# Performance work log

Measured on AMD Instinct MI355X. Metric: run time of the kernel, lower is better.

Reference implementation:

```python
import jax, jax.numpy as jnp
import numpy as np

B, V, J = 1024, 6890, 24
P_FEAT = (J - 1) * 9  # 207 pose-blendshape features
SMPL_PARENTS = [-1, 0, 0, 0, 1, 2, 3, 4, 5, 6, 7, 8, 9, 9, 9, 12, 13, 14, 16, 17, 18, 19, 20, 21]


def setup_inputs() -> dict:
    key = jax.random.key(0)
    ks = jax.random.split(key, 7)
    return {
        "betas": jax.random.normal(ks[0], (B, 10), jnp.float32),
        "full_pose": jax.random.normal(ks[1], (B, 72), jnp.float32) * 0.3,
        "v_template": jax.random.normal(ks[2], (1, V, 3), jnp.float32),
        "shapedirs": jax.random.normal(ks[3], (V, 3, 10), jnp.float32) * 0.01,
        "posedirs": jax.random.normal(ks[4], (P_FEAT, V * 3), jnp.float32) * 0.01,
        "J_regressor": jax.nn.softmax(jax.random.normal(ks[5], (J, V), jnp.float32), axis=-1),
        "lbs_weights": jax.nn.softmax(jax.random.normal(ks[6], (V, J), jnp.float32) * 4.0, axis=-1),
        "parents": jnp.array(SMPL_PARENTS, dtype=jnp.int32),
    }


def batch_rodrigues(rot_vecs):
    # rot_vecs: [..., 3] axis-angle -> [..., 3, 3] rotation matrices
    angle = jnp.linalg.norm(rot_vecs + 1e-8, axis=-1, keepdims=True)  # [...,1]
    axis = rot_vecs / angle
    s = jnp.sin(angle)[..., None]
    c = jnp.cos(angle)[..., None]
    kx, ky, kz = axis[..., 0], axis[..., 1], axis[..., 2]
    zeros = jnp.zeros_like(kx)
    K = jnp.stack([zeros, -kz, ky, kz, zeros, -kx, -ky, kx, zeros], axis=-1)
    K = K.reshape(rot_vecs.shape[:-1] + (3, 3))
    eye = jnp.eye(3, dtype=rot_vecs.dtype)
    return eye + s * K + (1.0 - c) * (K @ K)


def reference(betas, full_pose, v_template, shapedirs, posedirs, J_regressor, lbs_weights, parents):
    p = [int(x) for x in np.asarray(jax.device_get(parents))]  # static kinematic tree
    b = betas.shape[0]

    # 1) shape blendshapes: minimal shape
    v_shaped = v_template + jnp.einsum("bl,vkl->bvk", betas, shapedirs)  # [B,V,3]

    # 2) rest joints
    J_rest = jnp.einsum("jv,bvk->bjk", J_regressor, v_shaped)  # [B,J,3]

    # 3) pose rotations + pose blendshapes
    rot_mats = batch_rodrigues(full_pose.reshape(b, J, 3))  # [B,J,3,3]
    eye = jnp.eye(3, dtype=rot_mats.dtype)
    pose_feature = (rot_mats[:, 1:] - eye).reshape(b, P_FEAT)  # [B,207]
    v_posed = v_shaped + (pose_feature @ posedirs).reshape(b, V, 3)

    # 4) kinematic chain (sequential composition over fixed 24 joints)
    rel_joints = J_rest.at[:, 1:].add(-J_rest[:, np.array(p[1:])])  # [B,J,3]
    Tm = jnp.zeros((b, J, 4, 4), dtype=rot_mats.dtype)
    Tm = Tm.at[:, :, :3, :3].set(rot_mats)
    Tm = Tm.at[:, :, :3, 3].set(rel_joints)
    Tm = Tm.at[:, :, 3, 3].set(1.0)
    chain = [Tm[:, 0]]
    for i in range(1, J):
        chain.append(chain[p[i]] @ Tm[:, i])
    transforms = jnp.stack(chain, axis=1)  # [B,J,4,4]

    J_posed = transforms[:, :, :3, 3]  # [B,J,3]

    # relative bone transforms: subtract rotated rest joints from translation
    RJ = jnp.einsum("bjmn,bjn->bjm", transforms[:, :, :3, :3], J_rest)
    A = transforms.at[:, :, :3, 3].add(-RJ)  # [B,J,4,4]

    # 5) linear blend skinning: per-vertex weighted transform then apply
    T = jnp.einsum("vj,bjmn->bvmn", lbs_weights, A)  # [B,V,4,4]
    verts = jnp.einsum("bvmn,bvn->bvm", T[:, :, :3, :3], v_posed) + T[:, :, :3, 3]

    return verts, J_posed, J_rest, A, v_shaped
```

## Files before the change

kernel.cpp:

```cpp
#include <hip/hip_runtime.h>
#include <hip/hip_bf16.h>

#define BDIM 1024
#define VDIM 6890
#define NJ   24
#define NCOL (VDIM*3)
#define KPAD 224
#define NPAD 20736
#define NB   8
#define VPAD 6912

#define OUT_VERTS   0
#define OUT_JPOSED  21166080
#define OUT_JREST   21239808
#define OUT_A       21313536
#define OUT_VSHAPED 21706752

#define SCRF_PDT    0
#define SCRF_PF     2322432
#define SCRF_JTJS   2437120

#define WSB_PDT   0u
#define WSB_PF    9289728u
#define WSB_JTJS  9748480u
#define WSB_WHI   9752064u
#define WSB_WLO   10194432u
#define WSB_AHI   10636800u
#define WSB_ALO   11685376u
#define WS_NEED   12733952u

typedef __hip_bfloat16 bf16;
typedef unsigned short ushort_t;
typedef __attribute__((ext_vector_type(8))) short  short8;
typedef __attribute__((ext_vector_type(4))) float  float4v;

__device__ __forceinline__ bf16  tob(float x) { return __float2bfloat16(x); }

__device__ __forceinline__ ushort_t bf16_rne(float x) {
    unsigned u = __builtin_bit_cast(unsigned, x);
    unsigned r = (u + 0x7FFFu + ((u >> 16) & 1u)) >> 16;
    return (ushort_t)r;
}
__device__ __forceinline__ float bf16_to_f(ushort_t h) {
    unsigned u = ((unsigned)h) << 16;
    return __builtin_bit_cast(float, u);
}

__global__ __launch_bounds__(256) void k_prep(const float* __restrict__ jreg,
        const float* __restrict__ vt, const float* __restrict__ sd,
        const float* __restrict__ lbs, float* __restrict__ jtjs,
        ushort_t* __restrict__ whi, ushort_t* __restrict__ wlo) {
    if (blockIdx.x >= 24) {
        if (!whi) return;
        int idx = (blockIdx.x - 24)*256 + threadIdx.x;
        if (idx >= VPAD*32) return;
        int v = idx >> 5, j = idx & 31;
        float x = (v < VDIM && j < 24) ? lbs[v*24 + j] : 0.f;
        ushort_t h = bf16_rne(x);
        whi[idx] = h;
        wlo[idx] = bf16_rne(x - bf16_to_f(h));
        return;
    }
    int j = blockIdx.x;
    int tid = threadIdx.x;
    float acc[33];
#pragma unroll
    for (int i = 0; i < 33; i++) acc[i] = 0.f;
    for (int v = tid; v < VDIM; v += 256) {
        float r = jreg[j*VDIM + v];
#pragma unroll
        for (int m = 0; m < 3; m++) {
            acc[m] += r * vt[v*3+m];
#pragma unroll
            for (int l = 0; l < 10; l++)
                acc[3 + m*10 + l] += r * sd[(v*3+m)*10 + l];
        }
    }
    __shared__ float red[4][33];
    int lane = tid & 63, wid = tid >> 6;
#pragma unroll
    for (int i = 0; i < 33; i++) {
        float x = acc[i];
        for (int off = 32; off > 0; off >>= 1) x += __shfl_down(x, off);
        if (lane == 0) red[wid][i] = x;
    }
    __syncthreads();
    if (tid < 33)
        jtjs[j*33 + tid] = red[0][tid] + red[1][tid] + red[2][tid] + red[3][tid];
}

__global__ __launch_bounds__(256) void k_transpose(const float* __restrict__ pd,
        bf16* __restrict__ pdt) {
    __shared__ bf16 tile[32][65];
    int nt = blockIdx.x * 64;
    int kt = blockIdx.y * 32;
    int t = threadIdx.x;
    for (int i = t; i < 32*64; i += 256) {
        int kk = i >> 6, nn = i & 63;
        int k = kt + kk, n = nt + nn;
        float v = 0.f;
        if (k < 207 && n < NCOL) v = pd[k*NCOL + n];
        tile[kk][nn] = tob(v);
    }
    __syncthreads();
    for (int i = t; i < 32*64; i += 256) {
        int kk = i & 31, nn = i >> 5;
        pdt[(nt + nn)*KPAD + kt + kk] = tile[kk][nn];
    }
}

__global__ __launch_bounds__(64) void k_pose(const float* __restrict__ betas,
        const float* __restrict__ pose, const int* __restrict__ parents,
        const float* __restrict__ jtjs, float* __restrict__ out,
        bf16* __restrict__ wspf, ushort_t* __restrict__ ahi,
        ushort_t* __restrict__ alo) {
    int b = blockIdx.x, t = threadIdx.x;
    __shared__ float R[24][9];
    __shared__ float jrest[24][3];
    __shared__ float rel[24][3];
    __shared__ float ch[24][12];
    __shared__ int par[24];
    if (t < 24) {
        par[t] = parents[t];
        float rx = pose[b*72 + t*3 + 0];
        float ry = pose[b*72 + t*3 + 1];
        float rz = pose[b*72 + t*3 + 2];
        float ax = rx + 1e-8f, ay = ry + 1e-8f, az = rz + 1e-8f;
        float angle = sqrtf(ax*ax + ay*ay + az*az);
        float inv = 1.0f / angle;
        float kx = rx*inv, ky = ry*inv, kz = rz*inv;
        float s = sinf(angle), c = cosf(angle);
        float t1 = 1.0f - c;
        float q = kx*kx + ky*ky + kz*kz;
        R[t][0] = 1.f + t1*(kx*kx - q);
        R[t][1] = -s*kz + t1*kx*ky;
        R[t][2] =  s*ky + t1*kx*kz;
        R[t][3] =  s*kz + t1*kx*ky;
        R[t][4] = 1.f + t1*(ky*ky - q);
        R[t][5] = -s*kx + t1*ky*kz;
        R[t][6] = -s*ky + t1*kx*kz;
        R[t][7] =  s*kx + t1*ky*kz;
        R[t][8] = 1.f + t1*(kz*kz - q);
    }
    __syncthreads();
    for (int i = t; i < KPAD; i += 64) {
        float pf = 0.f;
        if (i < 207) {
            int j = i/9 + 1, e = i - (j-1)*9;
            pf = R[j][e] - ((e == 0 || e == 4 || e == 8) ? 1.f : 0.f);
        }
        wspf[b*KPAD + i] = tob(pf);
    }
    for (int i = t; i < 72; i += 64) {
        int j = i/3, k = i - j*3;
        const float* JJ = &jtjs[j*33];
        float s = JJ[k];
#pragma unroll
        for (int l = 0; l < 10; l++) s += JJ[3 + k*10 + l] * betas[b*10 + l];
        jrest[j][k] = s;
        out[OUT_JREST + b*72 + i] = s;
    }
    __syncthreads();
    for (int i = t; i < 72; i += 64) {
        int j = i/3, k = i - j*3;
        rel[j][k] = jrest[j][k] - (j > 0 ? jrest[par[j]][k] : 0.f);
    }
    __syncthreads();
    if (t < 12) {
        int m = t >> 2, n = t & 3;
        ch[0][t] = (n < 3) ? R[0][m*3+n] : rel[0][m];
    }
    __syncthreads();
    for (int i = 1; i < 24; i++) {
        float val = 0.f;
        if (t < 12) {
            int m = t >> 2, n = t & 3;
            int p = par[i];
            if (n < 3)
                val = ch[p][m*4+0]*R[i][n] + ch[p][m*4+1]*R[i][3+n] + ch[p][m*4+2]*R[i][6+n];
            else
                val = ch[p][m*4+0]*rel[i][0] + ch[p][m*4+1]*rel[i][1]
                    + ch[p][m*4+2]*rel[i][2] + ch[p][m*4+3];
        }
        if (t < 12) ch[i][t] = val;
        __syncthreads();
    }
    for (int i = t; i < 72; i += 64) {
        int j = i/3, k = i - j*3;
        out[OUT_JPOSED + b*72 + i] = ch[j][k*4+3];
    }
    for (int i = t; i < 384; i += 64) {
        int j = i >> 4, e = i & 15, m = e >> 2, n = e & 3;
        float v;
        if (m < 3) {
            if (n < 3) v = ch[j][m*4+n];
            else v = ch[j][m*4+3] - (ch[j][m*4+0]*jrest[j][0] + ch[j][m*4+1]*jrest[j][1]
                                   + ch[j][m*4+2]*jrest[j][2]);
        } else v = (n == 3) ? 1.f : 0.f;
        out[OUT_A + b*384 + i] = v;
    }
    if (ahi) {
        for (int i = t; i < 512; i += 64) {
            int e = i >> 5, j = i & 31;
            float v = 0.f;
            if (j < 24 && e < 12) {
                int m = e >> 2, n = e & 3;
                if (n < 3) v = ch[j][m*4+n];
                else v = ch[j][m*4+3] - (ch[j][m*4+0]*jrest[j][0] + ch[j][m*4+1]*jrest[j][1]
                                       + ch[j][m*4+2]*jrest[j][2]);
            }
            ushort_t h = bf16_rne(v);
            ahi[b*512 + i] = h;
            alo[b*512 + i] = bf16_rne(v - bf16_to_f(h));
        }
    }
}

__global__ __launch_bounds__(256) void k_gemmlbs(const bf16* __restrict__ wspf,
        const bf16* __restrict__ wspdt, const float* __restrict__ betas,
        const float* __restrict__ sd, const float* __restrict__ vt,
        const ushort_t* __restrict__ whi, const ushort_t* __restrict__ wlo,
        const ushort_t* __restrict__ ahi, const ushort_t* __restrict__ alo,
        float* __restrict__ out) {
    __shared__ float dtile[32][260];
    const ushort_t* pf  = (const ushort_t*)wspf;
    const ushort_t* pdt = (const ushort_t*)wspdt;
    int tid  = threadIdx.x;
    int lane = tid & 63, wave = tid >> 6;
    int l15 = lane & 15, quad = lane >> 4;
    int m0 = blockIdx.y * 32;
    int v0 = blockIdx.x * 64;
    int cb = wave * 48;
    int colb = v0*3 + cb;

    {
        float4v acc[2][3] = {};
        for (int c = 0; c < 7; c++) {
            short8 a[2], bb[3];
#pragma unroll
            for (int mf = 0; mf < 2; mf++)
                a[mf] = *reinterpret_cast<const short8*>(pf + (m0 + mf*16 + l15)*KPAD + c*32 + quad*8);
#pragma unroll
            for (int nf = 0; nf < 3; nf++)
                bb[nf] = *reinterpret_cast<const short8*>(pdt + (colb + nf*16 + l15)*KPAD + c*32 + quad*8);
#pragma unroll
            for (int mf = 0; mf < 2; mf++)
#pragma unroll
                for (int nf = 0; nf < 3; nf++)
                    acc[mf][nf] = __builtin_amdgcn_mfma_f32_16x16x32_bf16(a[mf], bb[nf], acc[mf][nf], 0, 0, 0);
        }
#pragma unroll
        for (int nf = 0; nf < 3; nf++) {
            int c0 = cb + nf*16 + l15;
            int vv = c0 / 3, rr = c0 - vv*3;
            int ad = vv*4 + rr;
#pragma unroll
            for (int mf = 0; mf < 2; mf++)
#pragma unroll
                for (int r = 0; r < 4; r++)
                    dtile[mf*16 + quad*4 + r][ad] = acc[mf][nf][r];
        }
    }
    __syncthreads();

    int wv = __builtin_amdgcn_readfirstlane(wave);
    int v = v0 + lane;
    float* vsh = out + OUT_VSHAPED;
    if (v < VDIM) {
        float vtv[3];
#pragma unroll
        for (int m = 0; m < 3; m++) vtv[m] = vt[v*3 + m];
        float sdv[30];
#pragma unroll
        for (int i = 0; i < 30; i++) sdv[i] = sd[v*30 + i];
#pragma unroll 2
        for (int bb2 = 0; bb2 < 8; bb2++) {
            int b  = m0 + wv*8 + bb2;
            int bl = wv*8 + bb2;
            float vs[3];
#pragma unroll
            for (int m = 0; m < 3; m++) {
                float s = vtv[m];
#pragma unroll
                for (int l = 0; l < 10; l++) s += betas[b*10 + l] * sdv[m*10 + l];
                vs[m] = s;
            }
            float4v* slot = reinterpret_cast<float4v*>(&dtile[bl][lane*4]);
            float4v d = *slot;
            float4v vp;
            vp[0] = vs[0] + d[0]; vp[1] = vs[1] + d[1];
            vp[2] = vs[2] + d[2]; vp[3] = 0.f;
            *slot = vp;
            int base = b*NCOL + v*3;
#pragma unroll
            for (int n = 0; n < 3; n++) vsh[base + n] = vs[n];
        }
    }

    short8 bhi[4], blo[4];
#pragma unroll
    for (int nf = 0; nf < 4; nf++) {
        int vv = v0 + nf*16 + l15;
        bhi[nf] = *reinterpret_cast<const short8*>(whi + vv*32 + quad*8);
        blo[nf] = *reinterpret_cast<const short8*>(wlo + vv*32 + quad*8);
    }
    const ushort_t* ah = ahi + (size_t)(m0 + wv*8)*512 + l15*32 + quad*8;
    const ushort_t* al = alo + (size_t)(m0 + wv*8)*512 + l15*32 + quad*8;
#pragma unroll 1
    for (int g = 0; g < 2; g++) {
        short8 a_hi[4], a_lo[4];
#pragma unroll
        for (int k = 0; k < 4; k++) {
            a_hi[k] = *reinterpret_cast<const short8*>(ah + (size_t)(g*4 + k)*512);
            a_lo[k] = *reinterpret_cast<const short8*>(al + (size_t)(g*4 + k)*512);
        }
#pragma unroll
        for (int k = 0; k < 4; k++) {
            int bb2 = g*4 + k;
            int b  = m0 + wv*8 + bb2;
            int bl = wv*8 + bb2;
#pragma unroll
            for (int nf = 0; nf < 4; nf++) {
                float4v acc = {};
                acc = __builtin_amdgcn_mfma_f32_16x16x32_bf16(a_hi[k], bhi[nf], acc, 0, 0, 0);
                acc = __builtin_amdgcn_mfma_f32_16x16x32_bf16(a_lo[k], bhi[nf], acc, 0, 0, 0);
                acc = __builtin_amdgcn_mfma_f32_16x16x32_bf16(a_hi[k], blo[nf], acc, 0, 0, 0);
                int vl = nf*16 + l15;
                float4v vp = *reinterpret_cast<const float4v*>(&dtile[bl][vl*4]);
                if (quad < 3 && v0 + vl < VDIM) {
                    float o = acc[3] + acc[0]*vp[0] + acc[1]*vp[1] + acc[2]*vp[2];
                    out[(size_t)b*NCOL + (size_t)(v0 + vl)*3 + quad] = o;
                }
            }
        }
    }
}

__global__ __launch_bounds__(256) void k_posegemm(const bf16* __restrict__ wspf,
        const bf16* __restrict__ wspdt, float* __restrict__ dout) {
    const ushort_t* pf  = (const ushort_t*)wspf;
    const ushort_t* pdt = (const ushort_t*)wspdt;
    int lane = threadIdx.x & 63;
    int wave = threadIdx.x >> 6;
    int l15 = lane & 15, quad = lane >> 4;
    int m0 = blockIdx.y * 32;
    int n0 = blockIdx.x * 256 + wave * 64;
    float4v acc[2][4] = {};
    for (int c = 0; c < 7; c++) {
        short8 a[2], bb[4];
#pragma unroll
        for (int mf = 0; mf < 2; mf++)
            a[mf] = *reinterpret_cast<const short8*>(pf + (m0 + mf*16 + l15)*KPAD + c*32 + quad*8);
#pragma unroll
        for (int nf = 0; nf < 4; nf++)
            bb[nf] = *reinterpret_cast<const short8*>(pdt + (n0 + nf*16 + l15)*KPAD + c*32 + quad*8);
#pragma unroll
        for (int mf = 0; mf < 2; mf++)
#pragma unroll
            for (int nf = 0; nf < 4; nf++)
                acc[mf][nf] = __builtin_amdgcn_mfma_f32_16x16x32_bf16(a[mf], bb[nf], acc[mf][nf], 0, 0, 0);
    }
#pragma unroll
    for (int mf = 0; mf < 2; mf++)
#pragma unroll
        for (int nf = 0; nf < 4; nf++) {
            int col = n0 + nf*16 + l15;
            if (col < NCOL) {
#pragma unroll
                for (int r = 0; r < 4; r++) {
                    int row = m0 + mf*16 + quad*4 + r;
                    dout[row*NCOL + col] = acc[mf][nf][r];
                }
            }
        }
}

__global__ __launch_bounds__(256) void k_lbs(const float* __restrict__ betas,
        const float* __restrict__ sd, const float* __restrict__ vt,
        const float* __restrict__ lbs, const float* __restrict__ Amat,
        float* __restrict__ out) {
    int tid = threadIdx.x;
    int v = blockIdx.x*256 + tid;
    if (v >= VDIM) return;
    int b0 = blockIdx.y * NB;
    float w[24];
    {
        const float4v* W4 = reinterpret_cast<const float4v*>(lbs + v*24);
#pragma unroll
        for (int q = 0; q < 6; q++) {
            float4v x = W4[q];
#pragma unroll
            for (int e = 0; e < 4; e++) w[q*4+e] = x[e];
        }
    }
    float vtv[3];
#pragma unroll
    for (int m = 0; m < 3; m++) vtv[m] = vt[v*3 + m];
    float sdv[30];
#pragma unroll
    for (int i = 0; i < 30; i++) sdv[i] = sd[v*30 + i];
    float* vsh = out + OUT_VSHAPED;
#pragma unroll 1
    for (int bb = 0; bb < NB; bb++) {
        int b = b0 + bb;
        const float* __restrict__ Ab = Amat + (size_t)b*384;
        float T[12];
#pragma unroll
        for (int e = 0; e < 12; e++) T[e] = 0.f;
#pragma unroll
        for (int j = 0; j < 24; j++) {
#pragma unroll
            for (int e = 0; e < 12; e++)
                T[e] = fmaf(w[j], Ab[j*16 + e], T[e]);
        }
        float vs[3];
#pragma unroll
        for (int m = 0; m < 3; m++) {
            float s = vtv[m];
#pragma unroll
            for (int l = 0; l < 10; l++) s += betas[b*10 + l] * sdv[m*10 + l];
            vs[m] = s;
        }
        int base = b*NCOL + v*3;
        float vp0 = vs[0] + vsh[base + 0];
        float vp1 = vs[1] + vsh[base + 1];
        float vp2 = vs[2] + vsh[base + 2];
#pragma unroll
        for (int m = 0; m < 3; m++) {
            float o = T[m*4+3] + T[m*4]*vp0 + T[m*4+1]*vp1 + T[m*4+2]*vp2;
            out[base + m] = o;
            vsh[base + m] = vs[m];
        }
    }
}

extern "C" void kernel_launch(void* const* d_in, const int* in_sizes, int n_in,
                              void* d_out, int out_size, void* d_ws, size_t ws_size,
                              hipStream_t stream) {
    const float *betas = nullptr, *pose = nullptr, *vt = nullptr, *sd = nullptr,
                *pd = nullptr, *jreg = nullptr, *lbs = nullptr;
    const int* parents = nullptr;
    for (int i = 0; i < n_in; i++) {
        switch (in_sizes[i]) {
            case 10240:   betas = (const float*)d_in[i]; break;
            case 73728:   pose  = (const float*)d_in[i]; break;
            case 20670:   vt    = (const float*)d_in[i]; break;
            case 206700:  sd    = (const float*)d_in[i]; break;
            case 4278690: pd    = (const float*)d_in[i]; break;
            case 24:      parents = (const int*)d_in[i]; break;
            case 165360:
                if (!jreg) jreg = (const float*)d_in[i];
                else       lbs  = (const float*)d_in[i];
                break;
            default: break;
        }
    }
    float* out = (float*)d_out;
    if (d_ws && ws_size >= (size_t)WS_NEED) {
        bf16*     ws_pdt  = (bf16*)((char*)d_ws + WSB_PDT);
        bf16*     ws_pf   = (bf16*)((char*)d_ws + WSB_PF);
        float*    ws_jtjs = (float*)((char*)d_ws + WSB_JTJS);
        ushort_t* ws_whi  = (ushort_t*)((char*)d_ws + WSB_WHI);
        ushort_t* ws_wlo  = (ushort_t*)((char*)d_ws + WSB_WLO);
        ushort_t* ws_ahi  = (ushort_t*)((char*)d_ws + WSB_AHI);
        ushort_t* ws_alo  = (ushort_t*)((char*)d_ws + WSB_ALO);
        k_prep<<<888, 256, 0, stream>>>(jreg, vt, sd, lbs, ws_jtjs, ws_whi, ws_wlo);
        k_transpose<<<dim3(324, 7), 256, 0, stream>>>(pd, ws_pdt);
        k_pose<<<BDIM, 64, 0, stream>>>(betas, pose, parents, ws_jtjs, out, ws_pf,
                                        ws_ahi, ws_alo);
        k_gemmlbs<<<dim3(108, 32), 256, 0, stream>>>(ws_pf, ws_pdt, betas, sd, vt,
                                                     ws_whi, ws_wlo, ws_ahi, ws_alo, out);
    } else {
        bf16*  ws_pdt  = (bf16*)(out + SCRF_PDT);
        bf16*  ws_pf   = (bf16*)(out + SCRF_PF);
        float* ws_jtjs = out + SCRF_JTJS;
        k_prep<<<24, 256, 0, stream>>>(jreg, vt, sd, lbs, ws_jtjs, nullptr, nullptr);
        k_transpose<<<dim3(324, 7), 256, 0, stream>>>(pd, ws_pdt);
        k_pose<<<BDIM, 64, 0, stream>>>(betas, pose, parents, ws_jtjs, out, ws_pf,
                                        nullptr, nullptr);
        k_posegemm<<<dim3(81, 32), 256, 0, stream>>>(ws_pf, ws_pdt, out + OUT_VSHAPED);
        k_lbs<<<dim3(27, BDIM/NB), 256, 0, stream>>>(betas, sd, vt, lbs, out + OUT_A, out);
    }
}
```

Before: 304.0 us.

## Halve gemmlbs batch tile, merge prep and transpose kernels, vectorize transpose stores

Shrinks the batch tile of the fused pose-GEMM/LBS kernel from 32 to 16 rows, which doubles the grid and cuts per-block shared memory and registers. A launch-bounds hint asks for higher occupancy. The joint-regressor prep, LBS-weight split and posedirs transpose are merged into one launch to remove a kernel boundary. The transpose write-out now uses 16-byte vector stores. The smaller tile means each posedirs B fragment is reused by fewer batch rows, so more global loads are issued per unit of MFMA work.

New measurement: 326.5 us. 1.07x slower.

```diff
diff --git a/kernel.cpp b/kernel.cpp
--- a/kernel.cpp
+++ b/kernel.cpp
@@ -9,6 +9,7 @@
 #define NPAD 20736
 #define NB   8
 #define VPAD 6912
+#define MB   16
 
 #define OUT_VERTS   0
 #define OUT_JPOSED  21166080
@@ -46,14 +47,45 @@
     return __builtin_bit_cast(float, u);
 }
 
-__global__ __launch_bounds__(256) void k_prep(const float* __restrict__ jreg,
+__global__ __launch_bounds__(256) void k_prep2(const float* __restrict__ jreg,
         const float* __restrict__ vt, const float* __restrict__ sd,
-        const float* __restrict__ lbs, float* __restrict__ jtjs,
-        ushort_t* __restrict__ whi, ushort_t* __restrict__ wlo) {
-    if (blockIdx.x >= 24) {
+        const float* __restrict__ lbs, const float* __restrict__ pd,
+        float* __restrict__ jtjs, ushort_t* __restrict__ whi,
+        ushort_t* __restrict__ wlo, bf16* __restrict__ pdt) {
+    __shared__ float red[4][33];
+    __shared__ bf16 tile[32][65];
+    int bid = blockIdx.x;
+    int t = threadIdx.x;
+    if (bid < 24) {
+        int j = bid;
+        float acc[33];
+#pragma unroll
+        for (int i = 0; i < 33; i++) acc[i] = 0.f;
+        for (int v = t; v < VDIM; v += 256) {
+            float r = jreg[j*VDIM + v];
+#pragma unroll
+            for (int m = 0; m < 3; m++) {
+                acc[m] += r * vt[v*3+m];
+#pragma unroll
+                for (int l = 0; l < 10; l++)
+                    acc[3 + m*10 + l] += r * sd[(v*3+m)*10 + l];
+            }
+        }
+        int lane = t & 63, wid = t >> 6;
+#pragma unroll
+        for (int i = 0; i < 33; i++) {
+            float x = acc[i];
+            for (int off = 32; off > 0; off >>= 1) x += __shfl_down(x, off);
+            if (lane == 0) red[wid][i] = x;
+        }
+        __syncthreads();
+        if (t < 33)
+            jtjs[j*33 + t] = red[0][t] + red[1][t] + red[2][t] + red[3][t];
+        return;
+    }
+    if (bid < 888) {
         if (!whi) return;
-        int idx = (blockIdx.x - 24)*256 + threadIdx.x;
-        if (idx >= VPAD*32) return;
+        int idx = (bid - 24)*256 + t;
         int v = idx >> 5, j = idx & 31;
         float x = (v < VDIM && j < 24) ? lbs[v*24 + j] : 0.f;
         ushort_t h = bf16_rne(x);
@@ -61,40 +93,9 @@
         wlo[idx] = bf16_rne(x - bf16_to_f(h));
         return;
     }
-    int j = blockIdx.x;
-    int tid = threadIdx.x;
-    float acc[33];
-#pragma unroll
-    for (int i = 0; i < 33; i++) acc[i] = 0.f;
-    for (int v = tid; v < VDIM; v += 256) {
-        float r = jreg[j*VDIM + v];
-#pragma unroll
-        for (int m = 0; m < 3; m++) {
-            acc[m] += r * vt[v*3+m];
-#pragma unroll
-            for (int l = 0; l < 10; l++)
-                acc[3 + m*10 + l] += r * sd[(v*3+m)*10 + l];
-        }
-    }
-    __shared__ float red[4][33];
-    int lane = tid & 63, wid = tid >> 6;
-#pragma unroll
-    for (int i = 0; i < 33; i++) {
-        float x = acc[i];
-        for (int off = 32; off > 0; off >>= 1) x += __shfl_down(x, off);
-        if (lane == 0) red[wid][i] = x;
-    }
-    __syncthreads();
-    if (tid < 33)
-        jtjs[j*33 + tid] = red[0][tid] + red[1][tid] + red[2][tid] + red[3][tid];
-}
-
-__global__ __launch_bounds__(256) void k_transpose(const float* __restrict__ pd,
-        bf16* __restrict__ pdt) {
-    __shared__ bf16 tile[32][65];
-    int nt = blockIdx.x * 64;
-    int kt = blockIdx.y * 32;
-    int t = threadIdx.x;
+    int r = bid - 888;
+    int nt = (r % 324) * 64;
+    int kt = (r / 324) * 32;
     for (int i = t; i < 32*64; i += 256) {
         int kk = i >> 6, nn = i & 63;
         int k = kt + kk, n = nt + nn;
@@ -103,9 +104,13 @@
         tile[kk][nn] = tob(v);
     }
     __syncthreads();
-    for (int i = t; i < 32*64; i += 256) {
-        int kk = i & 31, nn = i >> 5;
-        pdt[(nt + nn)*KPAD + kt + kk] = tile[kk][nn];
+    {
+        int oct = t >> 6, nn = t & 63;
+        short8 o;
+#pragma unroll
+        for (int q = 0; q < 8; q++)
+            o[q] = (short)*reinterpret_cast<const ushort_t*>(&tile[oct*8 + q][nn]);
+        *reinterpret_cast<short8*>((ushort_t*)pdt + (nt + nn)*KPAD + kt + oct*8) = o;
     }
 }
 
@@ -216,38 +221,35 @@
     }
 }
 
-__global__ __launch_bounds__(256) void k_gemmlbs(const bf16* __restrict__ wspf,
+__global__ __launch_bounds__(256, 8) void k_gemmlbs(const bf16* __restrict__ wspf,
         const bf16* __restrict__ wspdt, const float* __restrict__ betas,
         const float* __restrict__ sd, const float* __restrict__ vt,
         const ushort_t* __restrict__ whi, const ushort_t* __restrict__ wlo,
         const ushort_t* __restrict__ ahi, const ushort_t* __restrict__ alo,
         float* __restrict__ out) {
-    __shared__ float dtile[32][260];
+    __shared__ float dtile[MB][260];
     const ushort_t* pf  = (const ushort_t*)wspf;
     const ushort_t* pdt = (const ushort_t*)wspdt;
     int tid  = threadIdx.x;
     int lane = tid & 63, wave = tid >> 6;
     int l15 = lane & 15, quad = lane >> 4;
-    int m0 = blockIdx.y * 32;
+    int m0 = blockIdx.y * MB;
     int v0 = blockIdx.x * 64;
     int cb = wave * 48;
     int colb = v0*3 + cb;
+    int wv = __builtin_amdgcn_readfirstlane(wave);
 
     {
-        float4v acc[2][3] = {};
+        float4v acc[3] = {};
         for (int c = 0; c < 7; c++) {
-            short8 a[2], bb[3];
-#pragma unroll
-            for (int mf = 0; mf < 2; mf++)
-                a[mf] = *reinterpret_cast<const short8*>(pf + (m0 + mf*16 + l15)*KPAD + c*32 + quad*8);
+            short8 a = *reinterpret_cast<const short8*>(pf + (m0 + l15)*KPAD + c*32 + quad*8);
+            short8 bb[3];
 #pragma unroll
             for (int nf = 0; nf < 3; nf++)
                 bb[nf] = *reinterpret_cast<const short8*>(pdt + (colb + nf*16 + l15)*KPAD + c*32 + quad*8);
 #pragma unroll
-            for (int mf = 0; mf < 2; mf++)
-#pragma unroll
-                for (int nf = 0; nf < 3; nf++)
-                    acc[mf][nf] = __builtin_amdgcn_mfma_f32_16x16x32_bf16(a[mf], bb[nf], acc[mf][nf], 0, 0, 0);
+            for (int nf = 0; nf < 3; nf++)
+                acc[nf] = __builtin_amdgcn_mfma_f32_16x16x32_bf16(a, bb[nf], acc[nf], 0, 0, 0);
         }
 #pragma unroll
         for (int nf = 0; nf < 3; nf++) {
@@ -255,15 +257,12 @@
             int vv = c0 / 3, rr = c0 - vv*3;
             int ad = vv*4 + rr;
 #pragma unroll
-            for (int mf = 0; mf < 2; mf++)
-#pragma unroll
-                for (int r = 0; r < 4; r++)
-                    dtile[mf*16 + quad*4 + r][ad] = acc[mf][nf][r];
-        }
-    }
-    __syncthreads();
-
-    int wv = __builtin_amdgcn_readfirstlane(wave);
+            for (int r = 0; r < 4; r++)
+                dtile[quad*4 + r][ad] = acc[nf][r];
+        }
+    }
+    __syncthreads();
+
     int v = v0 + lane;
     float* vsh = out + OUT_VSHAPED;
     if (v < VDIM) {
@@ -274,9 +273,9 @@
 #pragma unroll
         for (int i = 0; i < 30; i++) sdv[i] = sd[v*30 + i];
 #pragma unroll 2
-        for (int bb2 = 0; bb2 < 8; bb2++) {
-            int b  = m0 + wv*8 + bb2;
-            int bl = wv*8 + bb2;
+        for (int bb2 = 0; bb2 < 4; bb2++) {
+            int b  = m0 + wv*4 + bb2;
+            int bl = wv*4 + bb2;
             float vs[3];
 #pragma unroll
             for (int m = 0; m < 3; m++) {
@@ -304,33 +303,25 @@
         bhi[nf] = *reinterpret_cast<const short8*>(whi + vv*32 + quad*8);
         blo[nf] = *reinterpret_cast<const short8*>(wlo + vv*32 + quad*8);
     }
-    const ushort_t* ah = ahi + (size_t)(m0 + wv*8)*512 + l15*32 + quad*8;
-    const ushort_t* al = alo + (size_t)(m0 + wv*8)*512 + l15*32 + quad*8;
+    const ushort_t* ah = ahi + (size_t)(m0 + wv*4)*512 + l15*32 + quad*8;
+    const ushort_t* al = alo + (size_t)(m0 + wv*4)*512 + l15*32 + quad*8;
 #pragma unroll 1
-    for (int g = 0; g < 2; g++) {
-        short8 a_hi[4], a_lo[4];
-#pragma unroll
-        for (int k = 0; k < 4; k++) {
-            a_hi[k] = *reinterpret_cast<const short8*>(ah + (size_t)(g*4 + k)*512);
-            a_lo[k] = *reinterpret_cast<const short8*>(al + (size_t)(g*4 + k)*512);
-        }
-#pragma unroll
-        for (int k = 0; k < 4; k++) {
-            int bb2 = g*4 + k;
-            int b  = m0 + wv*8 + bb2;
-            int bl = wv*8 + bb2;
-#pragma unroll
-            for (int nf = 0; nf < 4; nf++) {
-                float4v acc = {};
-                acc = __builtin_amdgcn_mfma_f32_16x16x32_bf16(a_hi[k], bhi[nf], acc, 0, 0, 0);
-                acc = __builtin_amdgcn_mfma_f32_16x16x32_bf16(a_lo[k], bhi[nf], acc, 0, 0, 0);
-                acc = __builtin_amdgcn_mfma_f32_16x16x32_bf16(a_hi[k], blo[nf], acc, 0, 0, 0);
-                int vl = nf*16 + l15;
-                float4v vp = *reinterpret_cast<const float4v*>(&dtile[bl][vl*4]);
-                if (quad < 3 && v0 + vl < VDIM) {
-                    float o = acc[3] + acc[0]*vp[0] + acc[1]*vp[1] + acc[2]*vp[2];
-                    out[(size_t)b*NCOL + (size_t)(v0 + vl)*3 + quad] = o;
-                }
+    for (int bb2 = 0; bb2 < 4; bb2++) {
+        int b  = m0 + wv*4 + bb2;
+        int bl = wv*4 + bb2;
+        short8 a_hi = *reinterpret_cast<const short8*>(ah + (size_t)bb2*512);
+        short8 a_lo = *reinterpret_cast<const short8*>(al + (size_t)bb2*512);
+#pragma unroll
+        for (int nf = 0; nf < 4; nf++) {
+            float4v acc = {};
+            acc = __builtin_amdgcn_mfma_f32_16x16x32_bf16(a_hi, bhi[nf], acc, 0, 0, 0);
+            acc = __builtin_amdgcn_mfma_f32_16x16x32_bf16(a_lo, bhi[nf], acc, 0, 0, 0);
+            acc = __builtin_amdgcn_mfma_f32_16x16x32_bf16(a_hi, blo[nf], acc, 0, 0, 0);
+            int vl = nf*16 + l15;
+            float4v vp = *reinterpret_cast<const float4v*>(&dtile[bl][vl*4]);
+            if (quad < 3 && v0 + vl < VDIM) {
+                float o = acc[3] + acc[0]*vp[0] + acc[1]*vp[1] + acc[2]*vp[2];
+                out[(size_t)b*NCOL + (size_t)(v0 + vl)*3 + quad] = o;
             }
         }
     }
@@ -464,18 +455,18 @@
         ushort_t* ws_wlo  = (ushort_t*)((char*)d_ws + WSB_WLO);
         ushort_t* ws_ahi  = (ushort_t*)((char*)d_ws + WSB_AHI);
         ushort_t* ws_alo  = (ushort_t*)((char*)d_ws + WSB_ALO);
-        k_prep<<<888, 256, 0, stream>>>(jreg, vt, sd, lbs, ws_jtjs, ws_whi, ws_wlo);
-        k_transpose<<<dim3(324, 7), 256, 0, stream>>>(pd, ws_pdt);
+        k_prep2<<<3156, 256, 0, stream>>>(jreg, vt, sd, lbs, pd, ws_jtjs,
+                                          ws_whi, ws_wlo, ws_pdt);
         k_pose<<<BDIM, 64, 0, stream>>>(betas, pose, parents, ws_jtjs, out, ws_pf,
                                         ws_ahi, ws_alo);
-        k_gemmlbs<<<dim3(108, 32), 256, 0, stream>>>(ws_pf, ws_pdt, betas, sd, vt,
+        k_gemmlbs<<<dim3(108, BDIM/MB), 256, 0, stream>>>(ws_pf, ws_pdt, betas, sd, vt,
                                                      ws_whi, ws_wlo, ws_ahi, ws_alo, out);
     } else {
         bf16*  ws_pdt  = (bf16*)(out + SCRF_PDT);
         bf16*  ws_pf   = (bf16*)(out + SCRF_PF);
         float* ws_jtjs = out + SCRF_JTJS;
-        k_prep<<<24, 256, 0, stream>>>(jreg, vt, sd, lbs, ws_jtjs, nullptr, nullptr);
-        k_transpose<<<dim3(324, 7), 256, 0, stream>>>(pd, ws_pdt);
+        k_prep2<<<3156, 256, 0, stream>>>(jreg, vt, sd, lbs, pd, ws_jtjs,
+                                          nullptr, nullptr, ws_pdt);
         k_pose<<<BDIM, 64, 0, stream>>>(betas, pose, parents, ws_jtjs, out, ws_pf,
                                         nullptr, nullptr);
         k_posegemm<<<dim3(81, 32), 256, 0, stream>>>(ws_pf, ws_pdt, out + OUT_VSHAPED);
```
